# Kernel optimization log

Hardware: AMD Instinct MI355X
Metric: run time of the kernel (lower is better)

## Reference

```python
import jax, jax.numpy as jnp
import numpy as np
from jax import lax

B, T, C = 2, 1024, 2048
H, N = 32, 64
LAYER_ID, N_LAYER = 1, 24
EPS = 1e-5 * 64.0  # 1e-5 * head_size_divisor**2, divisor=8
RESCALE_T = 256.0 * 0.7  # bf16_limit * 0.7


def setup_inputs():
    key = jax.random.key(0)
    ks = jax.random.split(key, 16)
    r01 = LAYER_ID / (N_LAYER - 1)
    r10 = 1.0 - LAYER_ID / N_LAYER
    ddd = np.arange(C, dtype=np.float64) / C
    pw = lambda p: jnp.asarray(1.0 - ddd ** p, jnp.float32)
    n = np.arange(C, dtype=np.float64)
    decay = -7.0 + 5.0 * (n / (C - 1)) ** (0.85 + r01 ** 0.5)
    sc = lambda k, shp, s: jax.random.normal(k, shp, jnp.float32) * s
    return {
        'x': sc(ks[0], (B, T, C), 1.0),
        'v_first': sc(ks[1], (B, T, C), 1.0),
        'x_r': pw(0.2 * r10), 'x_w': pw(0.9 * r10),
        'x_k': jnp.asarray(1.0 - (ddd ** (0.9 * r10) + 0.4 * r01), jnp.float32),
        'x_v': jnp.asarray(1.0 - (ddd ** (0.4 * r10) + 0.6 * r01), jnp.float32),
        'x_a': pw(0.9 * r10), 'x_g': pw(0.2 * r10),
        'w0': jnp.asarray(decay + 0.5, jnp.float32),
        'w1': sc(ks[2], (C, 64), 0.02), 'w2': sc(ks[3], (64, C), 0.02),
        'a0': jnp.zeros((C,), jnp.float32),
        'a1': sc(ks[4], (C, 64), 0.02), 'a2': sc(ks[5], (64, C), 0.02),
        'v0': jnp.ones((C,), jnp.float32),
        'v1': sc(ks[6], (C, 32), 0.02), 'v2': sc(ks[7], (32, C), 0.02),
        'g1': sc(ks[8], (C, 128), 0.02), 'g2': sc(ks[9], (128, C), 0.02),
        'k_k': jnp.full((C,), 0.85, jnp.float32),
        'k_a': jnp.ones((C,), jnp.float32),
        'r_k': sc(ks[10], (H, N), 0.05),
        'W_r': sc(ks[11], (C, C), C ** -0.5),
        'W_k': sc(ks[12], (C, C), C ** -0.5),
        'W_v': sc(ks[13], (C, C), C ** -0.5),
        'W_o': sc(ks[14], (C, C), C ** -0.5),
        'ln_w': jnp.ones((C,), jnp.float32),
        'ln_b': jnp.zeros((C,), jnp.float32),
    }


def wkv7(r, w, k, v, a, b):
    # RWKV-7 per-head linear state recurrence: S <- S*diag(w) + S a b^T + v k^T; out = S r
    Bsz, Tlen, Cd = r.shape
    to = lambda t: t.reshape(Bsz, Tlen, H, N).transpose(1, 0, 2, 3)  # (T,B,H,N)
    rr, kk, vv, aa, bb = map(to, (r, k, v, a, b))
    ww = jnp.exp(-jnp.exp(to(w)))  # decay in (0,1); w <= -0.5 guaranteed upstream

    def step(S, xs):
        rt, wt, kt, vt, at, bt = xs
        sa = jnp.einsum('bhij,bhj->bhi', S, at)
        S = S * wt[:, :, None, :] + sa[..., None] * bt[:, :, None, :] + vt[..., None] * kt[:, :, None, :]
        return S, jnp.einsum('bhij,bhj->bhi', S, rt)

    S0 = jnp.zeros((Bsz, H, N, N), r.dtype)
    _, out = lax.scan(step, S0, (rr, ww, kk, vv, aa, bb))
    return out.transpose(1, 0, 2, 3).reshape(Bsz, Tlen, Cd)


def reference(x, v_first, x_r, x_w, x_k, x_v, x_a, x_g, w0, w1, w2, a0, a1, a2,
              v0, v1, v2, g1, g2, k_k, k_a, r_k, W_r, W_k, W_v, W_o, ln_w, ln_b):
    # token shift (ZeroPad2d((0,0,1,-1)))
    xx = jnp.concatenate([jnp.zeros_like(x[:, :1]), x[:, :-1]], axis=1) - x
    xr = x + xx * x_r; xw = x + xx * x_w; xk = x + xx * x_k
    xv = x + xx * x_v; xa = x + xx * x_a; xg = x + xx * x_g
    r = xr @ W_r.T
    w = -jax.nn.softplus(-(w0 + jnp.tanh(xw @ w1) @ w2)) - 0.5  # soft clamp to (-inf,-0.5]
    k = xk @ W_k.T
    v = xv @ W_v.T
    # layer_id > 0: value residual gated toward v_first (with max-abs rescales)
    v1p = xv @ v1
    v1p = v1p / jnp.maximum(jnp.max(jnp.abs(v1p)), 1.0)
    v2p = v1p @ v2
    v2p = v2p / jnp.maximum(jnp.max(jnp.abs(v2p)), 1.0)
    gate = jax.nn.sigmoid(jnp.clip(v0 + v2p, -16.0, 16.0))
    vd = v_first - v
    vd = vd / jnp.maximum(jnp.max(jnp.abs(vd)), 1.0)
    v = v + vd * gate
    a = jax.nn.sigmoid(a0 + (xa @ a1) @ a2)
    g = jax.nn.sigmoid(xg @ g1) @ g2
    kk = (k * k_k).reshape(B, T, H, N)
    kk = (kk / jnp.maximum(jnp.linalg.norm(kk, axis=-1, keepdims=True), 1e-12)).reshape(B, T, C)
    k = k * (1.0 + (a - 1.0) * k_a)
    y = wkv7(r, w, k, v, -kk, kk * a)
    needs_rescale = jnp.max(jnp.abs(y)) > RESCALE_T
    # GroupNorm: H groups of size N
    yg = y.reshape(B, T, H, N)
    mu = yg.mean(-1, keepdims=True)
    var = yg.var(-1, keepdims=True)
    y = ((yg - mu) / jnp.sqrt(var + EPS)).reshape(B, T, C) * ln_w + ln_b
    y = y + ((r.reshape(B, T, H, N) * k.reshape(B, T, H, N) * r_k).sum(-1, keepdims=True)
             * v.reshape(B, T, H, N)).reshape(B, T, C)
    y = (y * g) @ W_o.T
    y = jnp.where(needs_rescale, y * 0.5, y)
    v_first_out = jnp.where(needs_rescale, v_first * 0.5, v_first)
    return y, v_first_out
```

## Files before the change

### kernel.cpp

```cpp
#include <hip/hip_runtime.h>
#include <hip/hip_bf16.h>

#define ELq 4194304
#define Cq 2048
#define Tq 1024
#define Hq 32
#define Mq 2048
#define SBYTES 1536

typedef __attribute__((ext_vector_type(8))) short bf16x8;
typedef __attribute__((ext_vector_type(4))) float f32x4;

__device__ __forceinline__ unsigned short f2bu(float f) {
  union { float f; unsigned u; } v; v.f = f;
  unsigned r = v.u + 0x7fffu + ((v.u >> 16) & 1u);
  return (unsigned short)(r >> 16);
}
__device__ __forceinline__ float b2f(unsigned short u) {
  union { unsigned u; float f; } v; v.u = ((unsigned)u) << 16;
  return v.f;
}
__device__ __forceinline__ void gl_lds16(const void* g, void* l) {
  __builtin_amdgcn_global_load_lds((const __attribute__((address_space(1))) unsigned int*)g,
                                   (__attribute__((address_space(3))) unsigned int*)l, 16, 0, 0);
}

template<int CTRL>
__device__ __forceinline__ float dpp_add(float x) {
  int t = __builtin_amdgcn_update_dpp(0, __builtin_bit_cast(int, x), CTRL, 0xF, 0xF, true);
  return x + __builtin_bit_cast(float, t);
}

__device__ __forceinline__ size_t sb_off(int m, int c) {
  size_t blk = (size_t)(((m >> 10) * 32 + (c >> 6)) * 1024 + (m & 1023));
  return blk * SBYTES;
}

struct ConvJob { const float* src; unsigned short* dst; int rows, cols, trans; };
struct ConvJobs { ConvJob j[12]; unsigned int* scal; };

__global__ void k_conv(ConvJobs jobs) {
  if (blockIdx.z == 0 && blockIdx.x == 0 && threadIdx.x < 8) jobs.scal[threadIdx.x] = 0u;
  ConvJob jb = jobs.j[blockIdx.z];
  int n = jb.rows * jb.cols;
  if (!jb.trans) {
    int n4 = n >> 2;
    for (int i = blockIdx.x * blockDim.x + threadIdx.x; i < n4; i += gridDim.x * blockDim.x) {
      float4 v = ((const float4*)jb.src)[i];
      ushort4 o;
      o.x = f2bu(v.x); o.y = f2bu(v.y); o.z = f2bu(v.z); o.w = f2bu(v.w);
      ((ushort4*)jb.dst)[i] = o;
    }
  } else {
    for (int i = blockIdx.x * blockDim.x + threadIdx.x; i < n; i += gridDim.x * blockDim.x) {
      int col = i / jb.rows;
      int row = i - col * jb.rows;
      jb.dst[i] = f2bu(jb.src[(size_t)row * jb.cols + col]);
    }
  }
}

__global__ void k_prologue(const float* __restrict__ x,
    const float* __restrict__ mr, const float* __restrict__ mw, const float* __restrict__ mk,
    const float* __restrict__ mv, const float* __restrict__ ma, const float* __restrict__ mg,
    unsigned short* __restrict__ xr, unsigned short* __restrict__ xw, unsigned short* __restrict__ xk,
    unsigned short* __restrict__ xv, unsigned short* __restrict__ xa, unsigned short* __restrict__ xg)
{
  int i4 = blockIdx.x * 256 + threadIdx.x;
  if (i4 >= ELq / 4) return;
  int i = i4 << 2;
  float4 xc = *(const float4*)(x + i);
  int t = (i >> 11) & (Tq - 1);
  float4 xp = make_float4(0.f, 0.f, 0.f, 0.f);
  if (t) xp = *(const float4*)(x + i - Cq);
  float4 dx = make_float4(xp.x - xc.x, xp.y - xc.y, xp.z - xc.z, xp.w - xc.w);
  int c = i & (Cq - 1);
  auto mix = [&](const float* __restrict__ m, unsigned short* __restrict__ o) {
    float4 mm = *(const float4*)(m + c);
    ushort4 u;
    u.x = f2bu(xc.x + dx.x * mm.x); u.y = f2bu(xc.y + dx.y * mm.y);
    u.z = f2bu(xc.z + dx.z * mm.z); u.w = f2bu(xc.w + dx.w * mm.w);
    *(ushort4*)(o + i) = u;
  };
  mix(mr, xr); mix(mw, xw); mix(mk, xk); mix(mv, xv); mix(ma, xa); mix(mg, xg);
}

struct GJob {
  const unsigned short* A; const unsigned short* B;
  const float* bias; float* Cf; unsigned short* Cb;
  unsigned int* amax; const float* aux;
  int K; int ld; int epi;
  const float* kkw; const float* kaw; const float* asig;
  unsigned char* scan;
};
struct GJobs { GJob j[4]; };

__device__ __forceinline__ void epi_store(int epi, float v, size_t o,
    float* Cf, unsigned short* Cb, const float* bias, int col, float& lmax)
{
  switch (epi) {
    case 0: Cf[o] = v; break;
    case 1: Cf[o] = v + bias[col]; break;
    case 2: Cf[o] = 1.f / (1.f + expf(-(v + bias[col]))); break;
    case 4: Cb[o] = f2bu(v); break;
    case 7: lmax = fmaxf(lmax, fabsf(v)); Cf[o] = v; break;
  }
}

__global__ __launch_bounds__(256, 2) void k_gemm128(GJobs jobs) {
  GJob jb = jobs.j[blockIdx.z];
  __shared__ __align__(16) unsigned short As[2][128 * 32];
  __shared__ __align__(16) unsigned short Bs[2][128 * 32];
  __shared__ float sred[4];
  const int tid = threadIdx.x, lane = tid & 63, wid = tid >> 6;
  const int wr = wid >> 1, wc = wid & 1;
  const int lin = blockIdx.y * 16 + blockIdx.x;
  const int swz = (lin & 7) * 32 + (lin >> 3);
  const int m0 = (swz >> 4) * 128, n0 = (swz & 15) * 128;
  const int K = jb.K, ld = jb.ld;
  const unsigned short* A = jb.A; const unsigned short* B = jb.B;
  f32x4 acc[4][4] = {};
  const int stg_row = (wid * 64 + lane) >> 2;
  const int stg_q   = lane & 3;
  const int stg_row2 = stg_row + 64;
  for (int k0 = 0; k0 < K; k0 += 64) {
    const bool h2 = (k0 + 32 < K);
    {
      int cw0 = wid * 64, cw1 = wid * 64 + 256;
      gl_lds16(A + (size_t)(m0 + stg_row) * ld + k0 + stg_q * 8, &As[0][cw0 * 8]);
      gl_lds16(B + (size_t)(n0 + stg_row) * ld + k0 + stg_q * 8, &Bs[0][cw0 * 8]);
      gl_lds16(A + (size_t)(m0 + stg_row2) * ld + k0 + stg_q * 8, &As[0][cw1 * 8]);
      gl_lds16(B + (size_t)(n0 + stg_row2) * ld + k0 + stg_q * 8, &Bs[0][cw1 * 8]);
      if (h2) {
        gl_lds16(A + (size_t)(m0 + stg_row) * ld + k0 + 32 + stg_q * 8, &As[1][cw0 * 8]);
        gl_lds16(B + (size_t)(n0 + stg_row) * ld + k0 + 32 + stg_q * 8, &Bs[1][cw0 * 8]);
        gl_lds16(A + (size_t)(m0 + stg_row2) * ld + k0 + 32 + stg_q * 8, &As[1][cw1 * 8]);
        gl_lds16(B + (size_t)(n0 + stg_row2) * ld + k0 + 32 + stg_q * 8, &Bs[1][cw1 * 8]);
      }
    }
    __syncthreads();
    const int kg = (lane >> 4) * 8;
    bf16x8 af[4], bq[4];
    #pragma unroll
    for (int mi = 0; mi < 4; ++mi)
      af[mi] = *(const bf16x8*)&As[0][(wr * 64 + mi * 16 + (lane & 15)) * 32 + kg];
    #pragma unroll
    for (int ni = 0; ni < 4; ++ni)
      bq[ni] = *(const bf16x8*)&Bs[0][(wc * 64 + ni * 16 + (lane & 15)) * 32 + kg];
    #pragma unroll
    for (int mi = 0; mi < 4; ++mi)
      #pragma unroll
      for (int ni = 0; ni < 4; ++ni)
        acc[mi][ni] = __builtin_amdgcn_mfma_f32_16x16x32_bf16(af[mi], bq[ni], acc[mi][ni], 0, 0, 0);
    if (h2) {
      #pragma unroll
      for (int mi = 0; mi < 4; ++mi)
        af[mi] = *(const bf16x8*)&As[1][(wr * 64 + mi * 16 + (lane & 15)) * 32 + kg];
      #pragma unroll
      for (int ni = 0; ni < 4; ++ni)
        bq[ni] = *(const bf16x8*)&Bs[1][(wc * 64 + ni * 16 + (lane & 15)) * 32 + kg];
      #pragma unroll
      for (int mi = 0; mi < 4; ++mi)
        #pragma unroll
        for (int ni = 0; ni < 4; ++ni)
          acc[mi][ni] = __builtin_amdgcn_mfma_f32_16x16x32_bf16(af[mi], bq[ni], acc[mi][ni], 0, 0, 0);
    }
    __syncthreads();
  }
  if (jb.epi == 12) {
    #pragma unroll
    for (int mi = 0; mi < 4; ++mi)
      #pragma unroll
      for (int ni = 0; ni < 4; ++ni) {
        int col = n0 + wc * 64 + ni * 16 + (lane & 15);
        int row0 = m0 + wr * 64 + mi * 16 + ((lane >> 4) << 2);
        #pragma unroll
        for (int q = 0; q < 4; ++q)
          *(float*)(jb.scan + sb_off(row0 + q, col) + ((col & 63) << 2)) = acc[mi][ni][q];
      }
    return;
  }
  if (jb.epi == 10) {
    #pragma unroll
    for (int mi = 0; mi < 4; ++mi)
      #pragma unroll
      for (int ni = 0; ni < 4; ++ni) {
        int col = n0 + wc * 64 + ni * 16 + (lane & 15);
        int row0 = m0 + wr * 64 + mi * 16 + ((lane >> 4) << 2);
        float bc = jb.bias[col];
        #pragma unroll
        for (int q = 0; q < 4; ++q) {
          float wv = acc[mi][ni][q] + bc;
          float wlog = -log1pf(expf(-wv)) - 0.5f;
          *(float*)(jb.scan + sb_off(row0 + q, col) + 1024 + ((col & 63) << 2)) =
              expf(-expf(wlog));
        }
      }
    return;
  }
  if (jb.epi == 11) {
    float kkwv[4], kawv[4]; int colv[4];
    #pragma unroll
    for (int ni = 0; ni < 4; ++ni) {
      colv[ni] = n0 + wc * 64 + ni * 16 + (lane & 15);
      kkwv[ni] = jb.kkw[colv[ni]];
      kawv[ni] = jb.kaw[colv[ni]];
    }
    #pragma unroll
    for (int mi = 0; mi < 4; ++mi) {
      #pragma unroll
      for (int q = 0; q < 4; ++q) {
        float kkv[4]; float ss = 0.f;
        #pragma unroll
        for (int ni = 0; ni < 4; ++ni) {
          kkv[ni] = acc[mi][ni][q] * kkwv[ni];
          ss += kkv[ni] * kkv[ni];
        }
        ss = dpp_add<0xB1>(ss); ss = dpp_add<0x4E>(ss);
        ss = dpp_add<0x141>(ss); ss = dpp_add<0x140>(ss);
        float inv = 1.f / fmaxf(sqrtf(ss), 1e-12f);
        int row = m0 + wr * 64 + mi * 16 + ((lane >> 4) << 2) + q;
        #pragma unroll
        for (int ni = 0; ni < 4; ++ni) {
          int col = colv[ni];
          unsigned char* base = jb.scan + sb_off(row, col);
          int n4 = (col & 63) << 2;
          float kraw = acc[mi][ni][q];
          float kkn = kkv[ni] * inv;
          float as = jb.asig[(size_t)row * 2048 + col];
          *(float*)(base + 256 + n4) = kraw * (1.f + (as - 1.f) * kawv[ni]);
          *(float*)(base + 512 + n4) = -kkn;
          *(float*)(base + 768 + n4) = kkn * as;
        }
      }
    }
    return;
  }
  float lmax = 0.f;
  if (jb.epi == 9) {
    #pragma unroll
    for (int mi = 0; mi < 4; ++mi)
      #pragma unroll
      for (int ni = 0; ni < 4; ++ni) {
        int col = n0 + wc * 64 + ni * 16 + (lane & 15);
        int row0 = m0 + wr * 64 + mi * 16 + ((lane >> 4) << 2);
        #pragma unroll
        for (int q = 0; q < 4; ++q) {
          float v = acc[mi][ni][q];
          lmax = fmaxf(lmax, fabsf(jb.aux[(size_t)(row0 + q) * 2048 + col] - v));
          *(float*)(jb.scan + sb_off(row0 + q, col) + 1280 + ((col & 63) << 2)) = v;
        }
      }
  } else {
    #pragma unroll
    for (int mi = 0; mi < 4; ++mi)
      #pragma unroll
      for (int ni = 0; ni < 4; ++ni) {
        int col = n0 + wc * 64 + ni * 16 + (lane & 15);
        int row = m0 + wr * 64 + mi * 16 + ((lane >> 4) << 2);
        #pragma unroll
        for (int q = 0; q < 4; ++q)
          epi_store(jb.epi, acc[mi][ni][q], (size_t)(row + q) * 2048 + col,
                    jb.Cf, jb.Cb, jb.bias, col, lmax);
      }
  }
  if (jb.epi == 7 || jb.epi == 9) {
    #pragma unroll
    for (int o = 32; o; o >>= 1) lmax = fmaxf(lmax, __shfl_xor(lmax, o));
    if (lane == 0) sred[wid] = lmax;
    __syncthreads();
    if (tid == 0)
      atomicMax(jb.amax, __float_as_uint(fmaxf(fmaxf(sred[0], sred[1]), fmaxf(sred[2], sred[3]))));
  }
}

template<int TBN>
__device__ __forceinline__ void sk_body(const GJob& jb,
    unsigned short* __restrict__ As, unsigned short* __restrict__ Bs) {
  const int tid = threadIdx.x, lane = tid & 63, wid = tid >> 6;
  const int m0 = blockIdx.x * 128;
  const int koff = blockIdx.y * 256;
  const int ld = jb.ld;
  constexpr int NF = TBN / 16;
  const unsigned short* A = jb.A + koff;
  const unsigned short* B = jb.B + koff;
  float* out = jb.Cf + (size_t)blockIdx.y * (2048 * TBN);
  f32x4 acc[2][NF] = {};
  for (int k0 = 0; k0 < 256; k0 += 32) {
    for (int cw = wid * 64; cw < 512; cw += 256) {
      int c = cw + lane; int row = c >> 2, q = c & 3;
      gl_lds16(A + (size_t)(m0 + row) * ld + k0 + q * 8, &As[cw * 8]);
    }
    for (int cw = wid * 64; cw < TBN * 4; cw += 256) {
      int c = cw + lane; int row = c >> 2, q = c & 3;
      gl_lds16(B + (size_t)row * ld + k0 + q * 8, &Bs[cw * 8]);
    }
    __syncthreads();
    const int kg = (lane >> 4) * 8;
    bf16x8 af[2], bq[NF];
    #pragma unroll
    for (int mi = 0; mi < 2; ++mi)
      af[mi] = *(const bf16x8*)&As[(wid * 32 + mi * 16 + (lane & 15)) * 32 + kg];
    #pragma unroll
    for (int ni = 0; ni < NF; ++ni)
      bq[ni] = *(const bf16x8*)&Bs[(ni * 16 + (lane & 15)) * 32 + kg];
    #pragma unroll
    for (int mi = 0; mi < 2; ++mi)
      #pragma unroll
      for (int ni = 0; ni < NF; ++ni)
        acc[mi][ni] = __builtin_amdgcn_mfma_f32_16x16x32_bf16(af[mi], bq[ni], acc[mi][ni], 0, 0, 0);
    __syncthreads();
  }
  #pragma unroll
  for (int mi = 0; mi < 2; ++mi)
    #pragma unroll
    for (int ni = 0; ni < NF; ++ni) {
      int col = ni * 16 + (lane & 15);
      int row = m0 + wid * 32 + mi * 16 + ((lane >> 4) << 2);
      #pragma unroll
      for (int q = 0; q < 4; ++q)
        out[(size_t)(row + q) * TBN + col] = acc[mi][ni][q];
    }
}

__global__ __launch_bounds__(256, 2) void k_skinny(GJobs jobs) {
  __shared__ __align__(16) unsigned short As[128 * 32];
  __shared__ __align__(16) unsigned short Bs[128 * 32];
  switch (blockIdx.z) {
    case 0:  sk_body<64>(jobs.j[0], As, Bs); break;
    case 1:  sk_body<64>(jobs.j[1], As, Bs); break;
    case 2:  sk_body<32>(jobs.j[2], As, Bs); break;
    default: sk_body<128>(jobs.j[3], As, Bs); break;
  }
}

__global__ void k_skepi(const float* __restrict__ pw, const float* __restrict__ pa,
                        const float* __restrict__ pv, const float* __restrict__ pg,
                        unsigned short* __restrict__ hw, unsigned short* __restrict__ ha,
                        unsigned short* __restrict__ hv, unsigned short* __restrict__ hg,
                        unsigned int* __restrict__ amax) {
  int i = blockIdx.x * 256 + threadIdx.x;
  const float* src; unsigned short* dst; int stride, mode, loc;
  if (i < 131072)      { src = pw; dst = hw; stride = 131072; mode = 0; loc = i; }
  else if (i < 262144) { src = pa; dst = ha; stride = 131072; mode = 1; loc = i - 131072; }
  else if (i < 327680) { src = pv; dst = hv; stride = 65536;  mode = 2; loc = i - 262144; }
  else                 { src = pg; dst = hg; stride = 262144; mode = 3; loc = i - 327680; }
  float s = 0.f;
  #pragma unroll
  for (int sp = 0; sp < 8; ++sp) s += src[loc + (size_t)sp * stride];
  float lmax = 0.f, o;
  switch (mode) {
    case 0: o = tanhf(s); break;
    case 1: o = s; break;
    case 2: o = s; lmax = fabsf(s); break;
    default: o = 1.f / (1.f + expf(-s)); break;
  }
  dst[loc] = f2bu(o);
  #pragma unroll
  for (int of = 32; of; of >>= 1) lmax = fmaxf(lmax, __shfl_xor(lmax, of));
  if ((threadIdx.x & 63) == 0 && lmax > 0.f) atomicMax(amax, __float_as_uint(lmax));
}

__global__ void k_vfin(const float* __restrict__ vf, const float* __restrict__ z,
                       const float* __restrict__ v0c, const unsigned int* __restrict__ sc,
                       unsigned char* __restrict__ scan) {
  int i4 = blockIdx.x * 256 + threadIdx.x;
  if (i4 >= ELq / 4) return;
  int i = i4 << 2;
  float m1 = fmaxf(__uint_as_float(sc[0]), 1.f);
  float m2 = fmaxf(__uint_as_float(sc[1]) / m1, 1.f);
  float inv12 = 1.f / (m1 * m2);
  float invvd = 1.f / fmaxf(__uint_as_float(sc[2]), 1.f);
  int m = i >> 11;
  int c = i & (Cq - 1);
  float* vp = (float*)(scan + sb_off(m, c) + 1280 + ((c & 63) << 2));
  float4 zv = *(const float4*)(z + i);
  float4 vv = *(const float4*)vp;
  float4 fv = *(const float4*)(vf + i);
  float4 v0v = *(const float4*)(v0c + c);
  float4 o;
  #pragma unroll
  for (int j = 0; j < 4; ++j) {
    float gx = (&v0v.x)[j] + (&zv.x)[j] * inv12;
    gx = fminf(fmaxf(gx, -16.f), 16.f);
    float gate = 1.f / (1.f + expf(-gx));
    float vr = (&vv.x)[j];
    (&o.x)[j] = vr + ((&fv.x)[j] - vr) * (gate * invvd);
  }
  *(float4*)vp = o;
}

struct SRg { float4 r, k, a, b, w; float v; };

__device__ __forceinline__ void ld_g(SRg& R, const unsigned char* p, int cl16, int row) {
  R.r = *(const float4*)(p + cl16);
  R.k = *(const float4*)(p + 256 + cl16);
  R.a = *(const float4*)(p + 512 + cl16);
  R.b = *(const float4*)(p + 768 + cl16);
  R.w = *(const float4*)(p + 1024 + cl16);
  R.v = *(const float*)(p + 1280 + row * 4);
}

__device__ __forceinline__ void wkv_step(const SRg& R, float S[4], float& ymx,
    float* __restrict__ y, size_t yoff, int lane) {
  float sa = (S[0]*R.a.x + S[1]*R.a.y) + (S[2]*R.a.z + S[3]*R.a.w);
  sa = dpp_add<0xB1>(sa);
  sa = dpp_add<0x4E>(sa);
  sa = dpp_add<0x141>(sa);
  sa = dpp_add<0x140>(sa);
  float vi = R.v;
  float s0 = S[0]*R.w.x + (sa*R.b.x + vi*R.k.x);
  float s1 = S[1]*R.w.y + (sa*R.b.y + vi*R.k.y);
  float s2 = S[2]*R.w.z + (sa*R.b.z + vi*R.k.z);
  float s3 = S[3]*R.w.w + (sa*R.b.w + vi*R.k.w);
  S[0]=s0; S[1]=s1; S[2]=s2; S[3]=s3;
  float yp = (s0*R.r.x + s1*R.r.y) + (s2*R.r.z + s3*R.r.w);
  yp = dpp_add<0xB1>(yp);
  yp = dpp_add<0x4E>(yp);
  yp = dpp_add<0x141>(yp);
  yp = dpp_add<0x140>(yp);
  if ((lane & 15) == 0) {
    y[yoff] = yp;
    ymx = fmaxf(ymx, fabsf(yp));
  }
}

__global__ __launch_bounds__(64, 1) void k_wkv(const unsigned char* __restrict__ scan,
    float* __restrict__ y, unsigned int* __restrict__ ymax) {
  const int lane = threadIdx.x;
  const int bh = blockIdx.x & 63;
  const int rq = blockIdx.x >> 6;
  const int row = rq * 4 + (lane >> 4);
  const int cl16 = (lane & 15) * 16;
  float S[4];
  #pragma unroll
  for (int q = 0; q < 4; ++q) S[q] = 0.f;
  const unsigned char* gs = scan + (size_t)bh * Tq * SBYTES;
  const size_t ybase = (size_t)(bh >> 5) * Tq * Cq + (size_t)(bh & 31) * 64 + row;

  SRg R0, R1, R2, R3, R4, R5, R6, R7;
  ld_g(R0, gs,              cl16, row);
  ld_g(R1, gs + SBYTES,     cl16, row);
  ld_g(R2, gs + 2 * SBYTES, cl16, row);
  ld_g(R3, gs + 3 * SBYTES, cl16, row);
  ld_g(R4, gs + 4 * SBYTES, cl16, row);
  ld_g(R5, gs + 5 * SBYTES, cl16, row);
  ld_g(R6, gs + 6 * SBYTES, cl16, row);
  ld_g(R7, gs + 7 * SBYTES, cl16, row);

  float ymx = 0.f;
  for (int t = 0; t < Tq; t += 8) {
    int n0 = (t + 8  < Tq) ? t + 8  : Tq - 1;
    int n1 = (t + 9  < Tq) ? t + 9  : Tq - 1;
    int n2 = (t + 10 < Tq) ? t + 10 : Tq - 1;
    int n3 = (t + 11 < Tq) ? t + 11 : Tq - 1;
    int n4 = (t + 12 < Tq) ? t + 12 : Tq - 1;
    int n5 = (t + 13 < Tq) ? t + 13 : Tq - 1;
    int n6 = (t + 14 < Tq) ? t + 14 : Tq - 1;
    int n7 = (t + 15 < Tq) ? t + 15 : Tq - 1;
    wkv_step(R0, S, ymx, y, ybase + (size_t)t * Cq, lane);
    ld_g(R0, gs + (size_t)n0 * SBYTES, cl16, row);
    wkv_step(R1, S, ymx, y, ybase + (size_t)(t + 1) * Cq, lane);
    ld_g(R1, gs + (size_t)n1 * SBYTES, cl16, row);
    wkv_step(R2, S, ymx, y, ybase + (size_t)(t + 2) * Cq, lane);
    ld_g(R2, gs + (size_t)n2 * SBYTES, cl16, row);
    wkv_step(R3, S, ymx, y, ybase + (size_t)(t + 3) * Cq, lane);
    ld_g(R3, gs + (size_t)n3 * SBYTES, cl16, row);
    wkv_step(R4, S, ymx, y, ybase + (size_t)(t + 4) * Cq, lane);
    ld_g(R4, gs + (size_t)n4 * SBYTES, cl16, row);
    wkv_step(R5, S, ymx, y, ybase + (size_t)(t + 5) * Cq, lane);
    ld_g(R5, gs + (size_t)n5 * SBYTES, cl16, row);
    wkv_step(R6, S, ymx, y, ybase + (size_t)(t + 6) * Cq, lane);
    ld_g(R6, gs + (size_t)n6 * SBYTES, cl16, row);
    wkv_step(R7, S, ymx, y, ybase + (size_t)(t + 7) * Cq, lane);
    ld_g(R7, gs + (size_t)n7 * SBYTES, cl16, row);
  }
  #pragma unroll
  for (int o = 32; o; o >>= 1) ymx = fmaxf(ymx, __shfl_xor(ymx, o));
  if (lane == 0) atomicMax(ymax, __float_as_uint(ymx));
}

__global__ __launch_bounds__(256) void k_epi1(const float* __restrict__ y,
    const unsigned char* __restrict__ scan, const unsigned short* __restrict__ g,
    const float* __restrict__ lnw, const float* __restrict__ lnb, const float* __restrict__ rk,
    unsigned short* __restrict__ yg) {
  int wid = threadIdx.x >> 6, lane = threadIdx.x & 63;
  int idx = blockIdx.x * 4 + wid;
  size_t off = (size_t)idx * 64 + lane;
  int c = ((idx & (Hq - 1)) << 6) | lane;
  int b = idx >> 15, t = (idx >> 5) & 1023, h = idx & 31;
  const unsigned char* so = scan + (size_t)((b * 32 + h) * 1024 + t) * SBYTES;
  float yv = y[off];
  float s = yv;
  #pragma unroll
  for (int o = 32; o; o >>= 1) s += __shfl_xor(s, o);
  float mu = s * (1.f / 64.f);
  float d = yv - mu;
  float vs = d * d;
  #pragma unroll
  for (int o = 32; o; o >>= 1) vs += __shfl_xor(vs, o);
  float yn = d / sqrtf(vs * (1.f / 64.f) + 6.4e-4f);
  float yo = yn * lnw[c] + lnb[c];
  float rv = *(const float*)(so + lane * 4);
  float kv = *(const float*)(so + 256 + lane * 4);
  float vv = *(const float*)(so + 1280 + lane * 4);
  float bon = rv * kv * rk[c];
  #pragma unroll
  for (int o = 32; o; o >>= 1) bon += __shfl_xor(bon, o);
  yo += bon * vv;
  yg[off] = f2bu(yo * b2f(g[off]));
}

__global__ void k_fin(const float* __restrict__ p0, const float* __restrict__ p1,
                      const unsigned int* __restrict__ sc, float* __restrict__ yout,
                      const float* __restrict__ vf, float* __restrict__ vfout) {
  int i = blockIdx.x * 256 + threadIdx.x;
  float s = (__uint_as_float(sc[3]) > 179.2f) ? 0.5f : 1.f;
  if (i < ELq / 4) {
    float4 a = ((const float4*)p0)[i];
    float4 b = ((const float4*)p1)[i];
    ((float4*)yout)[i] = make_float4((a.x + b.x) * s, (a.y + b.y) * s,
                                     (a.z + b.z) * s, (a.w + b.w) * s);
  } else {
    int j = i - ELq / 4;
    float4 vv = ((const float4*)vf)[j];
    ((float4*)vfout)[j] = make_float4(vv.x * s, vv.y * s, vv.z * s, vv.w * s);
  }
}

extern "C" void kernel_launch(void* const* d_in, const int* in_sizes, int n_in,
                              void* d_out, int out_size, void* d_ws, size_t ws_size,
                              hipStream_t stream) {
  const float* x      = (const float*)d_in[0];
  const float* vfirst = (const float*)d_in[1];
  const float* x_r = (const float*)d_in[2];
  const float* x_w = (const float*)d_in[3];
  const float* x_k = (const float*)d_in[4];
  const float* x_v = (const float*)d_in[5];
  const float* x_a = (const float*)d_in[6];
  const float* x_g = (const float*)d_in[7];
  const float* w0 = (const float*)d_in[8];
  const float* w1 = (const float*)d_in[9];
  const float* w2 = (const float*)d_in[10];
  const float* a0 = (const float*)d_in[11];
  const float* a1 = (const float*)d_in[12];
  const float* a2 = (const float*)d_in[13];
  const float* v0 = (const float*)d_in[14];
  const float* v1 = (const float*)d_in[15];
  const float* v2 = (const float*)d_in[16];
  const float* g1 = (const float*)d_in[17];
  const float* g2 = (const float*)d_in[18];
  const float* k_k = (const float*)d_in[19];
  const float* k_a = (const float*)d_in[20];
  const float* r_k = (const float*)d_in[21];
  const float* W_r = (const float*)d_in[22];
  const float* W_k = (const float*)d_in[23];
  const float* W_v = (const float*)d_in[24];
  const float* W_o = (const float*)d_in[25];
  const float* lnw = (const float*)d_in[26];
  const float* lnb = (const float*)d_in[27];

  char* ws = (char*)d_ws;
  size_t off = 0;
  auto alloc = [&](size_t bytes) -> void* {
    void* p = ws + off; off += (bytes + 255) & ~(size_t)255; return p;
  };
  unsigned int* scal = (unsigned int*)alloc(256);
  unsigned char* scanbuf = (unsigned char*)alloc((size_t)64 * Tq * SBYTES);
  unsigned short* xrb = (unsigned short*)alloc((size_t)ELq * 2);
  unsigned short* xwb = (unsigned short*)alloc((size_t)ELq * 2);
  unsigned short* xkb = (unsigned short*)alloc((size_t)ELq * 2);
  unsigned short* xvb = (unsigned short*)alloc((size_t)ELq * 2);
  unsigned short* xab = (unsigned short*)alloc((size_t)ELq * 2);
  unsigned short* xgb = (unsigned short*)alloc((size_t)ELq * 2);
  unsigned short* gbuf = (unsigned short*)alloc((size_t)ELq * 2);
  unsigned short* ygb  = (unsigned short*)alloc((size_t)ELq * 2);
  unsigned short* WrB = (unsigned short*)alloc((size_t)ELq * 2);
  unsigned short* WkB = (unsigned short*)alloc((size_t)ELq * 2);
  unsigned short* WvB = (unsigned short*)alloc((size_t)ELq * 2);
  unsigned short* WoB = (unsigned short*)alloc((size_t)ELq * 2);
  unsigned short* w1T = (unsigned short*)alloc(64 * 2048 * 2);
  unsigned short* a1T = (unsigned short*)alloc(64 * 2048 * 2);
  unsigned short* v1T = (unsigned short*)alloc(32 * 2048 * 2);
  unsigned short* g1T = (unsigned short*)alloc(128 * 2048 * 2);
  unsigned short* w2T = (unsigned short*)alloc(2048 * 64 * 2);
  unsigned short* a2T = (unsigned short*)alloc(2048 * 64 * 2);
  unsigned short* v2T = (unsigned short*)alloc(2048 * 32 * 2);
  unsigned short* g2T = (unsigned short*)alloc(2048 * 128 * 2);
  unsigned short* hwb = (unsigned short*)alloc((size_t)Mq * 64 * 2);
  unsigned short* hab = (unsigned short*)alloc((size_t)Mq * 64 * 2);
  unsigned short* hvb = (unsigned short*)alloc((size_t)Mq * 32 * 2);
  unsigned short* hgb = (unsigned short*)alloc((size_t)Mq * 128 * 2);
  float* pskw = (float*)alloc((size_t)8 * Mq * 64 * 4);
  float* pska = (float*)alloc((size_t)8 * Mq * 64 * 4);
  float* pskv = (float*)alloc((size_t)8 * Mq * 32 * 4);
  float* pskg = (float*)alloc((size_t)8 * Mq * 128 * 4);
  float* abuf = pskw;
  float* ybuf = (float*)xab;
  float* zbuf = (float*)d_out + ELq;
  float* yout = (float*)d_out;
  float* vfout = (float*)d_out + ELq;
  float* pWo0 = (float*)xrb;
  float* pWo1 = pWo0 + ELq;

  ConvJobs cj;
  cj.j[0]  = {W_r, WrB, Cq, Cq, 0};
  cj.j[1]  = {W_k, WkB, Cq, Cq, 0};
  cj.j[2]  = {W_v, WvB, Cq, Cq, 0};
  cj.j[3]  = {W_o, WoB, Cq, Cq, 0};
  cj.j[4]  = {w1, w1T, 2048, 64, 1};
  cj.j[5]  = {a1, a1T, 2048, 64, 1};
  cj.j[6]  = {v1, v1T, 2048, 32, 1};
  cj.j[7]  = {g1, g1T, 2048, 128, 1};
  cj.j[8]  = {w2, w2T, 64, 2048, 1};
  cj.j[9]  = {a2, a2T, 64, 2048, 1};
  cj.j[10] = {v2, v2T, 32, 2048, 1};
  cj.j[11] = {g2, g2T, 128, 2048, 1};
  cj.scal = scal;
  k_conv<<<dim3(1024, 1, 12), 256, 0, stream>>>(cj);

  k_prologue<<<ELq / 1024, 256, 0, stream>>>(x, x_r, x_w, x_k, x_v, x_a, x_g,
                                             xrb, xwb, xkb, xvb, xab, xgb);

  GJobs gsk;
  gsk.j[0] = {xwb, w1T, nullptr, pskw, nullptr, nullptr, nullptr, 256, 2048, 0};
  gsk.j[1] = {xab, a1T, nullptr, pska, nullptr, nullptr, nullptr, 256, 2048, 0};
  gsk.j[2] = {xvb, v1T, nullptr, pskv, nullptr, nullptr, nullptr, 256, 2048, 0};
  gsk.j[3] = {xgb, g1T, nullptr, pskg, nullptr, nullptr, nullptr, 256, 2048, 0};
  k_skinny<<<dim3(16, 8, 4), 256, 0, stream>>>(gsk);
  k_skepi<<<2304, 256, 0, stream>>>(pskw, pska, pskv, pskg, hwb, hab, hvb, hgb, scal + 0);

  GJobs g3j;
  g3j.j[0] = {hwb, w2T, w0, nullptr, nullptr, nullptr, nullptr, 64, 64, 10,
              nullptr, nullptr, nullptr, scanbuf};
  g3j.j[1] = {hab, a2T, a0, abuf, nullptr, nullptr, nullptr, 64, 64, 2};
  g3j.j[2] = {hvb, v2T, nullptr, zbuf, nullptr, scal + 1, nullptr, 32, 32, 7};
  g3j.j[3] = {hgb, g2T, nullptr, nullptr, gbuf, nullptr, nullptr, 128, 128, 4};
  k_gemm128<<<dim3(16, 16, 4), 256, 0, stream>>>(g3j);

  GJobs g1j;
  g1j.j[0] = {xrb, WrB, nullptr, nullptr, nullptr, nullptr, nullptr, 2048, 2048, 12,
              nullptr, nullptr, nullptr, scanbuf};
  g1j.j[1] = {xkb, WkB, nullptr, nullptr, nullptr, nullptr, nullptr, 2048, 2048, 11,
              k_k, k_a, abuf, scanbuf};
  g1j.j[2] = {xvb, WvB, nullptr, nullptr, nullptr, scal + 2, vfirst, 2048, 2048, 9,
              nullptr, nullptr, nullptr, scanbuf};
  g1j.j[3] = g1j.j[0];
  k_gemm128<<<dim3(16, 16, 3), 256, 0, stream>>>(g1j);

  k_vfin<<<ELq / 1024, 256, 0, stream>>>(vfirst, zbuf, v0, scal, scanbuf);
  k_wkv<<<16 * 2 * Hq, 64, 0, stream>>>(scanbuf, ybuf, scal + 3);
  k_epi1<<<(2 * Tq * Hq) / 4, 256, 0, stream>>>(ybuf, scanbuf, gbuf, lnw, lnb, r_k, ygb);

  GJobs gfj;
  gfj.j[0] = {ygb, WoB, nullptr, pWo0, nullptr, nullptr, nullptr, 1024, 2048, 0};
  gfj.j[1] = {ygb + 1024, WoB + 1024, nullptr, pWo1, nullptr, nullptr, nullptr, 1024, 2048, 0};
  gfj.j[2] = gfj.j[0]; gfj.j[3] = gfj.j[0];
  k_gemm128<<<dim3(16, 16, 2), 256, 0, stream>>>(gfj);
  k_fin<<<ELq / 512, 256, 0, stream>>>(pWo0, pWo1, scal, yout, vfirst, vfout);
}
```

Baseline: 478.2 us.

## Fuse pairs of WKV recurrence steps via precomputed two-step transition terms

Adds a parallel pre-pass kernel that, for each pair of timesteps, precomputes the composed decay, rank-one update vectors and readout vectors and their cross dot products. The sequential WKV scan then advances the state two steps per iteration, halving the serial dependency chain of reductions and state updates. It costs an extra kernel launch, extra memory traffic to write and read the pair buffer (reusing freed activation buffers, which are reordered in the allocation list), and changes floating-point summation order.

```diff
diff --git a/kernel.cpp b/kernel.cpp
--- a/kernel.cpp
+++ b/kernel.cpp
@@ -7,6 +7,7 @@
 #define Hq 32
 #define Mq 2048
 #define SBYTES 1536
+#define EBYTES 1664
 
 typedef __attribute__((ext_vector_type(8))) short bf16x8;
 typedef __attribute__((ext_vector_type(4))) float f32x4;
@@ -29,6 +30,11 @@
 __device__ __forceinline__ float dpp_add(float x) {
   int t = __builtin_amdgcn_update_dpp(0, __builtin_bit_cast(int, x), CTRL, 0xF, 0xF, true);
   return x + __builtin_bit_cast(float, t);
+}
+__device__ __forceinline__ float red16(float x) {
+  x = dpp_add<0xB1>(x); x = dpp_add<0x4E>(x);
+  x = dpp_add<0x141>(x); x = dpp_add<0x140>(x);
+  return x;
 }
 
 __device__ __forceinline__ size_t sb_off(int m, int c) {
@@ -216,8 +222,7 @@
           kkv[ni] = acc[mi][ni][q] * kkwv[ni];
           ss += kkv[ni] * kkv[ni];
         }
-        ss = dpp_add<0xB1>(ss); ss = dpp_add<0x4E>(ss);
-        ss = dpp_add<0x141>(ss); ss = dpp_add<0x140>(ss);
+        ss = red16(ss);
         float inv = 1.f / fmaxf(sqrtf(ss), 1e-12f);
         int row = m0 + wr * 64 + mi * 16 + ((lane >> 4) << 2) + q;
         #pragma unroll
@@ -390,42 +395,93 @@
   *(float4*)vp = o;
 }
 
-struct SRg { float4 r, k, a, b, w; float v; };
-
-__device__ __forceinline__ void ld_g(SRg& R, const unsigned char* p, int cl16, int row) {
-  R.r = *(const float4*)(p + cl16);
-  R.k = *(const float4*)(p + 256 + cl16);
-  R.a = *(const float4*)(p + 512 + cl16);
-  R.b = *(const float4*)(p + 768 + cl16);
-  R.w = *(const float4*)(p + 1024 + cl16);
-  R.v = *(const float*)(p + 1280 + row * 4);
-}
-
-__device__ __forceinline__ void wkv_step(const SRg& R, float S[4], float& ymx,
+__global__ __launch_bounds__(256) void k_pre2(const unsigned char* __restrict__ scan,
+                                              unsigned char* __restrict__ ext) {
+  const int wv = threadIdx.x >> 6, j = threadIdx.x & 63;
+  const int item = blockIdx.x * 4 + wv;
+  const int bh = item >> 9, p = item & 511;
+  const unsigned char* L1 = scan + ((size_t)bh * 1024 + 2 * p) * SBYTES;
+  const unsigned char* L2 = L1 + SBYTES;
+  auto ldf = [&](const unsigned char* b, int off) {
+    return *(const float*)(b + off + j * 4);
+  };
+  float r1 = ldf(L1, 0), k1 = ldf(L1, 256), a1 = ldf(L1, 512), b1 = ldf(L1, 768), w1 = ldf(L1, 1024);
+  float r2 = ldf(L2, 0), k2 = ldf(L2, 256), a2 = ldf(L2, 512), b2 = ldf(L2, 768), w2 = ldf(L2, 1024);
+  auto rsum = [](float x) {
+    #pragma unroll
+    for (int o = 32; o; o >>= 1) x += __shfl_xor(x, o);
+    return x;
+  };
+  float d_b1a2 = rsum(b1 * a2);
+  float d_k1a2 = rsum(k1 * a2);
+  float d_b1r1 = rsum(b1 * r1);
+  float d_k1r1 = rsum(k1 * r1);
+  float d_b2r2 = rsum(b2 * r2);
+  float d_k2r2 = rsum(k2 * r2);
+  float beta = b1 * w2 + d_b1a2 * b2;
+  float kap  = k1 * w2 + d_k1a2 * b2;
+  float alf  = w1 * a2;
+  float Wp   = w1 * w2;
+  float rho1 = w1 * r1 + d_b1r1 * a1;
+  float d_br2 = rsum(beta * r2);
+  float d_kr2 = rsum(kap * r2);
+  float rho2 = Wp * r2 + d_br2 * a1 + d_b2r2 * alf;
+  unsigned char* E = ext + (size_t)item * EBYTES;
+  *(float*)(E + 0    + j * 4) = alf;
+  *(float*)(E + 256  + j * 4) = beta;
+  *(float*)(E + 512  + j * 4) = kap;
+  *(float*)(E + 768  + j * 4) = Wp;
+  *(float*)(E + 1024 + j * 4) = rho1;
+  *(float*)(E + 1280 + j * 4) = rho2;
+  if (j == 0) {
+    float* s = (float*)(E + 1536);
+    s[0] = d_k1r1; s[1] = d_kr2; s[2] = d_k2r2; s[3] = 0.f;
+  }
+}
+
+struct SR2 { float4 a1, al, p1, p2, be, b2, ka, k2, Wp, sc; float v1, v2; };
+
+__device__ __forceinline__ void ld2(SR2& R, const unsigned char* L1,
+                                    const unsigned char* E, int cl16, int row) {
+  R.a1 = *(const float4*)(L1 + 512 + cl16);
+  R.k2 = *(const float4*)(L1 + SBYTES + 256 + cl16);
+  R.b2 = *(const float4*)(L1 + SBYTES + 768 + cl16);
+  R.v1 = *(const float*)(L1 + 1280 + row * 4);
+  R.v2 = *(const float*)(L1 + SBYTES + 1280 + row * 4);
+  R.al = *(const float4*)(E + 0    + cl16);
+  R.be = *(const float4*)(E + 256  + cl16);
+  R.ka = *(const float4*)(E + 512  + cl16);
+  R.Wp = *(const float4*)(E + 768  + cl16);
+  R.p1 = *(const float4*)(E + 1024 + cl16);
+  R.p2 = *(const float4*)(E + 1280 + cl16);
+  R.sc = *(const float4*)(E + 1536);
+}
+
+__device__ __forceinline__ float dot4(const float S[4], float4 v) {
+  return (S[0] * v.x + S[1] * v.y) + (S[2] * v.z + S[3] * v.w);
+}
+
+__device__ __forceinline__ void wkv_step2(const SR2& R, float S[4], float& ymx,
     float* __restrict__ y, size_t yoff, int lane) {
-  float sa = (S[0]*R.a.x + S[1]*R.a.y) + (S[2]*R.a.z + S[3]*R.a.w);
-  sa = dpp_add<0xB1>(sa);
-  sa = dpp_add<0x4E>(sa);
-  sa = dpp_add<0x141>(sa);
-  sa = dpp_add<0x140>(sa);
-  float vi = R.v;
-  float s0 = S[0]*R.w.x + (sa*R.b.x + vi*R.k.x);
-  float s1 = S[1]*R.w.y + (sa*R.b.y + vi*R.k.y);
-  float s2 = S[2]*R.w.z + (sa*R.b.z + vi*R.k.z);
-  float s3 = S[3]*R.w.w + (sa*R.b.w + vi*R.k.w);
-  S[0]=s0; S[1]=s1; S[2]=s2; S[3]=s3;
-  float yp = (s0*R.r.x + s1*R.r.y) + (s2*R.r.z + s3*R.r.w);
-  yp = dpp_add<0xB1>(yp);
-  yp = dpp_add<0x4E>(yp);
-  yp = dpp_add<0x141>(yp);
-  yp = dpp_add<0x140>(yp);
+  float sa1 = red16(dot4(S, R.a1));
+  float sa2 = red16(dot4(S, R.al));
+  float yr1 = red16(dot4(S, R.p1));
+  float yr2 = red16(dot4(S, R.p2));
+  float y1 = yr1 + R.sc.x * R.v1;
+  float y2 = yr2 + R.sc.y * R.v1 + R.sc.z * R.v2;
+  S[0] = S[0] * R.Wp.x + sa1 * R.be.x + sa2 * R.b2.x + R.v1 * R.ka.x + R.v2 * R.k2.x;
+  S[1] = S[1] * R.Wp.y + sa1 * R.be.y + sa2 * R.b2.y + R.v1 * R.ka.y + R.v2 * R.k2.y;
+  S[2] = S[2] * R.Wp.z + sa1 * R.be.z + sa2 * R.b2.z + R.v1 * R.ka.z + R.v2 * R.k2.z;
+  S[3] = S[3] * R.Wp.w + sa1 * R.be.w + sa2 * R.b2.w + R.v1 * R.ka.w + R.v2 * R.k2.w;
   if ((lane & 15) == 0) {
-    y[yoff] = yp;
-    ymx = fmaxf(ymx, fabsf(yp));
+    y[yoff] = y1;
+    y[yoff + Cq] = y2;
+    ymx = fmaxf(ymx, fmaxf(fabsf(y1), fabsf(y2)));
   }
 }
 
 __global__ __launch_bounds__(64, 1) void k_wkv(const unsigned char* __restrict__ scan,
+    const unsigned char* __restrict__ ext,
     float* __restrict__ y, unsigned int* __restrict__ ymax) {
   const int lane = threadIdx.x;
   const int bh = blockIdx.x & 63;
@@ -436,44 +492,29 @@
   #pragma unroll
   for (int q = 0; q < 4; ++q) S[q] = 0.f;
   const unsigned char* gs = scan + (size_t)bh * Tq * SBYTES;
+  const unsigned char* ge = ext + (size_t)bh * 512 * EBYTES;
   const size_t ybase = (size_t)(bh >> 5) * Tq * Cq + (size_t)(bh & 31) * 64 + row;
 
-  SRg R0, R1, R2, R3, R4, R5, R6, R7;
-  ld_g(R0, gs,              cl16, row);
-  ld_g(R1, gs + SBYTES,     cl16, row);
-  ld_g(R2, gs + 2 * SBYTES, cl16, row);
-  ld_g(R3, gs + 3 * SBYTES, cl16, row);
-  ld_g(R4, gs + 4 * SBYTES, cl16, row);
-  ld_g(R5, gs + 5 * SBYTES, cl16, row);
-  ld_g(R6, gs + 6 * SBYTES, cl16, row);
-  ld_g(R7, gs + 7 * SBYTES, cl16, row);
+  SR2 R0, R1, R2, R3;
+  ld2(R0, gs,                      ge,              cl16, row);
+  ld2(R1, gs + 2 * SBYTES,         ge + EBYTES,     cl16, row);
+  ld2(R2, gs + 4 * SBYTES,         ge + 2 * EBYTES, cl16, row);
+  ld2(R3, gs + 6 * SBYTES,         ge + 3 * EBYTES, cl16, row);
 
   float ymx = 0.f;
-  for (int t = 0; t < Tq; t += 8) {
-    int n0 = (t + 8  < Tq) ? t + 8  : Tq - 1;
-    int n1 = (t + 9  < Tq) ? t + 9  : Tq - 1;
-    int n2 = (t + 10 < Tq) ? t + 10 : Tq - 1;
-    int n3 = (t + 11 < Tq) ? t + 11 : Tq - 1;
-    int n4 = (t + 12 < Tq) ? t + 12 : Tq - 1;
-    int n5 = (t + 13 < Tq) ? t + 13 : Tq - 1;
-    int n6 = (t + 14 < Tq) ? t + 14 : Tq - 1;
-    int n7 = (t + 15 < Tq) ? t + 15 : Tq - 1;
-    wkv_step(R0, S, ymx, y, ybase + (size_t)t * Cq, lane);
-    ld_g(R0, gs + (size_t)n0 * SBYTES, cl16, row);
-    wkv_step(R1, S, ymx, y, ybase + (size_t)(t + 1) * Cq, lane);
-    ld_g(R1, gs + (size_t)n1 * SBYTES, cl16, row);
-    wkv_step(R2, S, ymx, y, ybase + (size_t)(t + 2) * Cq, lane);
-    ld_g(R2, gs + (size_t)n2 * SBYTES, cl16, row);
-    wkv_step(R3, S, ymx, y, ybase + (size_t)(t + 3) * Cq, lane);
-    ld_g(R3, gs + (size_t)n3 * SBYTES, cl16, row);
-    wkv_step(R4, S, ymx, y, ybase + (size_t)(t + 4) * Cq, lane);
-    ld_g(R4, gs + (size_t)n4 * SBYTES, cl16, row);
-    wkv_step(R5, S, ymx, y, ybase + (size_t)(t + 5) * Cq, lane);
-    ld_g(R5, gs + (size_t)n5 * SBYTES, cl16, row);
-    wkv_step(R6, S, ymx, y, ybase + (size_t)(t + 6) * Cq, lane);
-    ld_g(R6, gs + (size_t)n6 * SBYTES, cl16, row);
-    wkv_step(R7, S, ymx, y, ybase + (size_t)(t + 7) * Cq, lane);
-    ld_g(R7, gs + (size_t)n7 * SBYTES, cl16, row);
+  for (int p = 0; p < 512; p += 4) {
+    int n0 = (p + 4 < 512) ? p + 4 : 511;
+    int n1 = (p + 5 < 512) ? p + 5 : 511;
+    int n2 = (p + 6 < 512) ? p + 6 : 511;
+    int n3 = (p + 7 < 512) ? p + 7 : 511;
+    wkv_step2(R0, S, ymx, y, ybase + (size_t)(2 * p) * Cq, lane);
+    ld2(R0, gs + (size_t)(2 * n0) * SBYTES, ge + (size_t)n0 * EBYTES, cl16, row);
+    wkv_step2(R1, S, ymx, y, ybase + (size_t)(2 * p + 2) * Cq, lane);
+    ld2(R1, gs + (size_t)(2 * n1) * SBYTES, ge + (size_t)n1 * EBYTES, cl16, row);
+    wkv_step2(R2, S, ymx, y, ybase + (size_t)(2 * p + 4) * Cq, lane);
+    ld2(R2, gs + (size_t)(2 * n2) * SBYTES, ge + (size_t)n2 * EBYTES, cl16, row);
+    wkv_step2(R3, S, ymx, y, ybase + (size_t)(2 * p + 6) * Cq, lane);
+    ld2(R3, gs + (size_t)(2 * n3) * SBYTES, ge + (size_t)n3 * EBYTES, cl16, row);
   }
   #pragma unroll
   for (int o = 32; o; o >>= 1) ymx = fmaxf(ymx, __shfl_xor(ymx, o));
@@ -568,16 +609,10 @@
   unsigned int* scal = (unsigned int*)alloc(256);
   unsigned char* scanbuf = (unsigned char*)alloc((size_t)64 * Tq * SBYTES);
   unsigned short* xrb = (unsigned short*)alloc((size_t)ELq * 2);
-  unsigned short* xwb = (unsigned short*)alloc((size_t)ELq * 2);
-  unsigned short* xkb = (unsigned short*)alloc((size_t)ELq * 2);
-  unsigned short* xvb = (unsigned short*)alloc((size_t)ELq * 2);
   unsigned short* xab = (unsigned short*)alloc((size_t)ELq * 2);
   unsigned short* xgb = (unsigned short*)alloc((size_t)ELq * 2);
   unsigned short* gbuf = (unsigned short*)alloc((size_t)ELq * 2);
   unsigned short* ygb  = (unsigned short*)alloc((size_t)ELq * 2);
-  unsigned short* WrB = (unsigned short*)alloc((size_t)ELq * 2);
-  unsigned short* WkB = (unsigned short*)alloc((size_t)ELq * 2);
-  unsigned short* WvB = (unsigned short*)alloc((size_t)ELq * 2);
   unsigned short* WoB = (unsigned short*)alloc((size_t)ELq * 2);
   unsigned short* w1T = (unsigned short*)alloc(64 * 2048 * 2);
   unsigned short* a1T = (unsigned short*)alloc(64 * 2048 * 2);
@@ -591,12 +626,19 @@
   unsigned short* hab = (unsigned short*)alloc((size_t)Mq * 64 * 2);
   unsigned short* hvb = (unsigned short*)alloc((size_t)Mq * 32 * 2);
   unsigned short* hgb = (unsigned short*)alloc((size_t)Mq * 128 * 2);
+  unsigned short* xwb = (unsigned short*)alloc((size_t)ELq * 2);
+  unsigned short* xkb = (unsigned short*)alloc((size_t)ELq * 2);
+  unsigned short* xvb = (unsigned short*)alloc((size_t)ELq * 2);
+  unsigned short* WrB = (unsigned short*)alloc((size_t)ELq * 2);
+  unsigned short* WkB = (unsigned short*)alloc((size_t)ELq * 2);
+  unsigned short* WvB = (unsigned short*)alloc((size_t)ELq * 2);
   float* pskw = (float*)alloc((size_t)8 * Mq * 64 * 4);
   float* pska = (float*)alloc((size_t)8 * Mq * 64 * 4);
   float* pskv = (float*)alloc((size_t)8 * Mq * 32 * 4);
   float* pskg = (float*)alloc((size_t)8 * Mq * 128 * 4);
   float* abuf = pskw;
   float* ybuf = (float*)xab;
+  unsigned char* pairext = (unsigned char*)xwb;
   float* zbuf = (float*)d_out + ELq;
   float* yout = (float*)d_out;
   float* vfout = (float*)d_out + ELq;
@@ -649,7 +691,8 @@
   k_gemm128<<<dim3(16, 16, 3), 256, 0, stream>>>(g1j);
 
   k_vfin<<<ELq / 1024, 256, 0, stream>>>(vfirst, zbuf, v0, scal, scanbuf);
-  k_wkv<<<16 * 2 * Hq, 64, 0, stream>>>(scanbuf, ybuf, scal + 3);
+  k_pre2<<<(64 * 512) / 4, 256, 0, stream>>>(scanbuf, pairext);
+  k_wkv<<<16 * 2 * Hq, 64, 0, stream>>>(scanbuf, pairext, ybuf, scal + 3);
   k_epi1<<<(2 * Tq * Hq) / 4, 256, 0, stream>>>(ybuf, scanbuf, gbuf, lnw, lnb, r_k, ygb);
 
   GJobs gfj;
```

Measured after the change: 491.3 us. +2.7%, slower.
